# Kernel optimization log

Measured on AMD Instinct MI355X. Metric: run time of the kernel, lower is better.

## Reference

```python
import jax, jax.numpy as jnp
import numpy as np

PAD = 0  # pad_token_id sentinel used for word_starts and labels_arcs masking


def setup_inputs() -> dict:
    B, S, H, L = 16, 256, 768, 37
    key = jax.random.key(0)
    k1, k2, k3, k4, k5 = jax.random.split(key, 5)
    hidden = jax.random.normal(k1, (B, S, H), dtype=jnp.float32)
    # strictly-increasing subword start indices (1,3,5,...), zero-padded to S
    n_starts = S // 2
    row = jnp.concatenate([
        1 + 2 * jnp.arange(n_starts, dtype=jnp.int32),
        jnp.zeros(S - n_starts, dtype=jnp.int32),
    ])
    word_starts = jnp.tile(row[None, :], (B, 1))
    n_words = n_starts - 1  # spans are between consecutive starts
    la = jax.random.randint(k2, (B, S), 1, 2 * S, dtype=jnp.int32)
    labels_arcs = jnp.where(jnp.arange(S)[None, :] < n_words, la, PAD)
    labels_rels = jax.random.randint(k3, (B, S), 0, L, dtype=jnp.int32)
    W_arc = jax.random.normal(k4, (H + 1, H), dtype=jnp.float32) * 0.02
    W_rel = jax.random.normal(k5, (L, H + 1, H + 1), dtype=jnp.float32) * 0.02
    return dict(hidden=hidden, W_arc=W_arc, W_rel=W_rel,
                word_starts=word_starts, labels_arcs=labels_arcs,
                labels_rels=labels_rels)


def _merge_subword_tokens(hidden, word_starts):
    """Fused segment-mean: word j = mean(hidden[start_j:start_{j+1}])."""
    B, S, H = hidden.shape
    csum = jnp.concatenate(
        [jnp.zeros((B, 1, H), hidden.dtype), jnp.cumsum(hidden, axis=1)], axis=1)
    n_valid = jnp.sum(word_starts != PAD, axis=1)  # [B]
    start = word_starts  # [B,S]
    end = jnp.concatenate(
        [word_starts[:, 1:], jnp.zeros((B, 1), word_starts.dtype)], axis=1)
    valid = (jnp.arange(S)[None, :] + 1) < n_valid[:, None]  # word j needs start j+1
    s0 = jnp.take_along_axis(csum, start[..., None].astype(jnp.int32), axis=1)
    s1 = jnp.take_along_axis(csum, end[..., None].astype(jnp.int32), axis=1)
    length = jnp.clip(end - start, 1, None).astype(hidden.dtype)[..., None]
    return jnp.where(valid[..., None], (s1 - s0) / length, 0.0)  # [B,S,H]


def _with_ones(x):
    return jnp.concatenate([x, jnp.ones_like(x[..., :1])], axis=-1)


def reference(hidden, W_arc, W_rel, word_starts, labels_arcs, labels_rels):
    deps = _merge_subword_tokens(hidden, word_starts)            # [B,S,H]
    heads = jnp.concatenate([hidden, deps], axis=1)              # [B,2S,H]
    xa = _with_ones(deps)                                        # [B,S,H+1]
    arc_preds = jnp.einsum('bxi,ij,byj->bxy', xa, W_arc, heads)  # [B,S,2S]
    yr = _with_ones(heads)                                       # [B,2S,H+1]
    rel_preds = jnp.einsum('bxi,oij,byj->bxyo', xa, W_rel, yr)   # [B,S,2S,L]

    B, S, Y, L = rel_preds.shape
    mask = (labels_arcs != PAD).astype(hidden.dtype)             # [B,S]
    n = jnp.sum(mask)
    arc_lp = jax.nn.log_softmax(arc_preds, axis=-1)
    safe_arcs = jnp.clip(labels_arcs, 0, Y - 1)
    arc_ll = jnp.take_along_axis(arc_lp, safe_arcs[..., None], axis=-1)[..., 0]
    arc_loss = -jnp.sum(arc_ll * mask) / n

    idx = jnp.broadcast_to(safe_arcs[:, :, None, None], (B, S, 1, L))
    rel_sel = jnp.take_along_axis(rel_preds, idx, axis=2)[:, :, 0, :]  # [B,S,L]
    rel_lp = jax.nn.log_softmax(rel_sel, axis=-1)
    rel_ll = jnp.take_along_axis(rel_lp, labels_rels[..., None], axis=-1)[..., 0]
    rel_loss = -jnp.sum(rel_ll * mask) / n

    loss = arc_loss + rel_loss
    return loss, rel_preds, arc_preds
```

## Files before the change

### kernel.cpp

```cpp
#include <hip/hip_runtime.h>
#include <cmath>
#include <cstdint>


#define NB 16
#define SS 256
#define HH 768
#define LLn 37
#define YY 512
#define KP 800
#define JR 768

static const long long REL_ELEMS = (long long)NB * SS * YY * LLn;

typedef __bf16 bf16_t;
typedef __bf16 bf16x8 __attribute__((ext_vector_type(8)));
typedef float f32x4 __attribute__((ext_vector_type(4)));

__device__ __forceinline__ void async_copy16(const void* g, void* l) {
  __builtin_amdgcn_global_load_lds((__attribute__((address_space(1))) void*)(g),
                                   (__attribute__((address_space(3))) void*)(l),
                                   16, 0, 0);
}


__global__ void count_valid(const int* __restrict__ word_starts,
                            int* __restrict__ n_valid, float* __restrict__ lossacc) {
  __shared__ int cnt;
  if (threadIdx.x == 0) cnt = 0;
  __syncthreads();
  const int b = blockIdx.x;
  if (word_starts[b * SS + threadIdx.x] != 0) atomicAdd(&cnt, 1);
  __syncthreads();
  if (threadIdx.x == 0) {
    n_valid[b] = cnt;
    if (b == 0) { lossacc[0] = 0.f; lossacc[1] = 0.f; }
  }
}

__global__ void hid_rows(const float* __restrict__ hidden, bf16_t* __restrict__ yrb) {
  const long long r = blockIdx.x;
  const int b = (int)(r >> 8), y = (int)(r & 255);
  const float* src = hidden + r * HH;
  bf16_t* dst = yrb + ((long long)b * YY + y) * KP;
  const int t = threadIdx.x;
  for (int h = t; h < HH; h += 256) dst[h] = (bf16_t)src[h];
  if (t < KP - HH) dst[HH + t] = (t == 0) ? (bf16_t)1.0f : (bf16_t)0.0f;
}

__global__ void build_deps(const float* __restrict__ hidden, const int* __restrict__ word_starts,
                           const int* __restrict__ n_valid,
                           bf16_t* __restrict__ xa_p, bf16_t* __restrict__ yrb) {
  const int x = blockIdx.x, b = blockIdx.y, t = threadIdx.x;
  const int nv = n_valid[b];
  const bool valid = (x + 1) < nv;
  int start = word_starts[b * SS + x];
  int end = (x + 1 < SS) ? word_starts[b * SS + x + 1] : 0;
  start = min(max(start, 0), SS); end = min(max(end, 0), SS);
  const int len = max(end - start, 1);
  const float inv = 1.0f / (float)len;
  const float* hb = hidden + (long long)b * SS * HH;
  bf16_t* xr = xa_p + (long long)(b * SS + x) * KP;
  bf16_t* yr = yrb + ((long long)b * YY + SS + x) * KP;
  for (int h = t; h < HH; h += 256) {
    float s = 0.f;
    if (valid) for (int tt = start; tt < end; ++tt) s += hb[(long long)tt * HH + h];
    const bf16_t bv = (bf16_t)(valid ? s * inv : 0.f);
    xr[h] = bv; yr[h] = bv;
  }
  if (t < KP - HH) {
    const bf16_t v = (t == 0) ? (bf16_t)1.0f : (bf16_t)0.0f;
    xr[HH + t] = v; yr[HH + t] = v;
  }
}

__global__ void conv_warc(const float* __restrict__ W, bf16_t* __restrict__ Wab) {
  __shared__ float tbuf[32][33];
  const int i0 = blockIdx.x * 32, j0 = blockIdx.y * 32;
  const int tx = threadIdx.x, ty = threadIdx.y;
  for (int rr = 0; rr < 32; rr += 8) {
    const int i = i0 + ty + rr, j = j0 + tx;
    tbuf[ty + rr][tx] = (i < HH + 1) ? W[(long long)i * HH + j] : 0.f;
  }
  __syncthreads();
  for (int rr = 0; rr < 32; rr += 8) {
    const int j = j0 + ty + rr, i = i0 + tx;
    Wab[(long long)j * KP + i] = (bf16_t)tbuf[tx][ty + rr];
  }
}

__global__ void conv_wrel(const float* __restrict__ W, bf16_t* __restrict__ Wb, int o0) {
  __shared__ float tbuf[32][33];
  const int o = o0 + blockIdx.z;
  const int i0 = blockIdx.x * 32, j0 = blockIdx.y * 32;
  const int tx = threadIdx.x, ty = threadIdx.y;
  const float* Wo = W + (long long)o * (HH + 1) * (HH + 1);
  for (int rr = 0; rr < 32; rr += 8) {
    const int i = i0 + ty + rr, j = j0 + tx;
    tbuf[ty + rr][tx] = (i < HH + 1) ? Wo[(long long)i * (HH + 1) + j] : 0.f;
  }
  __syncthreads();
  bf16_t* Wbo = Wb + (long long)blockIdx.z * JR * KP;
  for (int rr = 0; rr < 32; rr += 8) {
    const int j = j0 + ty + rr, i = i0 + tx;
    Wbo[(long long)j * KP + i] = (bf16_t)tbuf[tx][ty + rr];
  }
}

__global__ void build_wb768(const float* __restrict__ W, bf16_t* __restrict__ Wb768) {
  const int o = blockIdx.x;
  bf16_t* dst = Wb768 + (long long)o * KP;
  for (int i = threadIdx.x; i < KP; i += 256) {
    float v = 0.f;
    if (o < LLn && i < HH + 1)
      v = W[(long long)o * (HH + 1) * (HH + 1) + (long long)i * (HH + 1) + HH];
    dst[i] = (bf16_t)v;
  }
}


template<int MODE>
__global__ __launch_bounds__(256)
void gemm_bt(const bf16_t* __restrict__ A, long long sAz, int lda,
             const bf16_t* __restrict__ B, long long sBz, int ldb,
             int K,
             float* __restrict__ Cf, bf16_t* __restrict__ Cb,
             long long sCz, int ldc,
             int OC, int o0, const float* __restrict__ bias2) {
  __shared__ __align__(16) char smem_raw[16896];
  bf16_t* As = (bf16_t*)smem_raw;
  bf16_t* Bs = (bf16_t*)(smem_raw + 8192);
  const int tid = threadIdx.x;
  const int w = tid >> 6;
  const int lane = tid & 63;
  const int z = blockIdx.z;
  const long long row0 = (long long)blockIdx.y * 128;
  const long long col0 = (long long)blockIdx.x * 128;
  const bf16_t* Ab = A + z * sAz + row0 * lda;
  const bf16_t* Bb = B + z * sBz + col0 * ldb;

  const int r_in = lane >> 2;
  const int kofs = (lane & 3) * 8;
  const bf16_t* gA0 = Ab + (long long)(w * 32 + r_in) * lda + kofs;
  const bf16_t* gB0 = Bb + (long long)(w * 32 + r_in) * ldb + kofs;
  const bf16_t* gA1 = gA0 + 16ll * lda;
  const bf16_t* gB1 = gB0 + 16ll * ldb;
  bf16_t* lA0 = &As[(w * 32) * 32];
  bf16_t* lA1 = &As[(w * 32 + 16) * 32];
  bf16_t* lB0 = &Bs[(w * 32) * 32];
  bf16_t* lB1 = &Bs[(w * 32 + 16) * 32];

  f32x4 acc[4][4];
  #pragma unroll
  for (int i = 0; i < 4; i++)
    #pragma unroll
    for (int j = 0; j < 4; j++)
      #pragma unroll
      for (int e = 0; e < 4; e++) acc[i][j][e] = 0.f;

  const int wm = (w >> 1) * 64, wn = (w & 1) * 64;
  const int fr = lane & 15;
  const int fq = lane >> 4;
  const int aoff = fq * 8;

  for (int k0 = 0; k0 < K; k0 += 32) {
    async_copy16(gA0 + k0, lA0);
    async_copy16(gA1 + k0, lA1);
    async_copy16(gB0 + k0, lB0);
    async_copy16(gB1 + k0, lB1);
    __syncthreads();
    bf16x8 af[4], bfr[4];
    #pragma unroll
    for (int t = 0; t < 4; t++) af[t]  = *(const bf16x8*)&As[(wm + t * 16 + fr) * 32 + aoff];
    #pragma unroll
    for (int t = 0; t < 4; t++) bfr[t] = *(const bf16x8*)&Bs[(wn + t * 16 + fr) * 32 + aoff];
    #pragma unroll
    for (int tm = 0; tm < 4; tm++)
      #pragma unroll
      for (int tn = 0; tn < 4; tn++)
        acc[tm][tn] = __builtin_amdgcn_mfma_f32_16x16x32_bf16(af[tm], bfr[tn], acc[tm][tn], 0, 0, 0);
    __syncthreads();
  }

  if (MODE == 2) {
    float* ebuf = (float*)smem_raw;
    const int c = tid & 127;
    const int rgrp = tid >> 7;
    const int n = (int)col0 + c;
    const int x = n / OC;
    const int o = o0 + (n - x * OC);
    const float bias = bias2[(((long long)z << 8) + x) * 128 + o];
    float* outp = Cf + z * sCz + (long long)x * (YY * LLn) + o;
    #pragma unroll
    for (int ch = 0; ch < 4; ch++) {
      #pragma unroll
      for (int tn = 0; tn < 4; tn++)
        #pragma unroll
        for (int e = 0; e < 4; e++)
          ebuf[((w >> 1) * 16 + fq * 4 + e) * 132 + wn + tn * 16 + fr] = acc[ch][tn][e];
      __syncthreads();
      const long long ybase = row0 + (long long)rgrp * 64 + ch * 16;
      #pragma unroll
      for (int r = 0; r < 16; r++)
        outp[(ybase + r) * LLn] = ebuf[(rgrp * 16 + r) * 132 + c] + bias;
      __syncthreads();
    }
  } else {
    const int er = fq * 4;
    #pragma unroll
    for (int tm = 0; tm < 4; tm++) {
      #pragma unroll
      for (int tn = 0; tn < 4; tn++) {
        const int rl = wm + tm * 16 + er;
        const long long col = col0 + wn + tn * 16 + fr;
        if (MODE == 0) {
          bf16_t* dst = Cb + z * sCz + col;
          #pragma unroll
          for (int r = 0; r < 4; r++)
            dst[(row0 + rl + r) * (long long)ldc] = (bf16_t)acc[tm][tn][r];
        } else {
          float* dst = Cf + z * sCz + col;
          #pragma unroll
          for (int r = 0; r < 4; r++)
            dst[(row0 + rl + r) * (long long)ldc] = acc[tm][tn][r];
        }
      }
    }
  }
}


__device__ __forceinline__ float wave_max(float v) {
  #pragma unroll
  for (int off = 32; off > 0; off >>= 1) v = fmaxf(v, __shfl_xor(v, off));
  return v;
}
__device__ __forceinline__ float wave_sum(float v) {
  #pragma unroll
  for (int off = 32; off > 0; off >>= 1) v += __shfl_xor(v, off);
  return v;
}

__global__ void loss_kernel(const float* __restrict__ arc, const float* __restrict__ rel,
                            const int* __restrict__ la, const int* __restrict__ lr,
                            float* __restrict__ acc) {
  const int r = blockIdx.x;
  const int lane = threadIdx.x;
  const int lab = la[r];
  const float* ar = arc + (long long)r * YY;
  float v[8]; float m = -INFINITY;
  #pragma unroll
  for (int i = 0; i < 8; i++) { v[i] = ar[lane + 64 * i]; m = fmaxf(m, v[i]); }
  m = wave_max(m);
  float s = 0.f;
  #pragma unroll
  for (int i = 0; i < 8; i++) s += expf(v[i] - m);
  s = wave_sum(s);
  const float lse_a = m + logf(s);
  const int safe = lab < 0 ? 0 : (lab > YY - 1 ? YY - 1 : lab);
  const float* rr = rel + ((long long)r * YY + safe) * LLn;
  const float rv = (lane < LLn) ? rr[lane] : -INFINITY;
  const float m2 = wave_max(rv);
  const float s2 = wave_sum((lane < LLn) ? expf(rv - m2) : 0.f);
  const float lse_r = m2 + logf(s2);
  if (lane == 0 && lab != 0) {
    const float ll = (ar[safe] - lse_a) + (rr[lr[r]] - lse_r);
    atomicAdd(&acc[0], ll);
    atomicAdd(&acc[1], 1.f);
  }
}

__global__ void finalize(const float* __restrict__ acc, float* __restrict__ out) {
  out[0] = -acc[0] / acc[1];
}


extern "C" void kernel_launch(void* const* d_in, const int* in_sizes, int n_in,
                              void* d_out, int out_size, void* d_ws, size_t ws_size,
                              hipStream_t stream) {
  (void)in_sizes; (void)n_in; (void)out_size;
  const float* hidden      = (const float*)d_in[0];
  const float* W_arc       = (const float*)d_in[1];
  const float* W_rel       = (const float*)d_in[2];
  const int* word_starts   = (const int*)d_in[3];
  const int* labels_arcs   = (const int*)d_in[4];
  const int* labels_rels   = (const int*)d_in[5];

  float* out = (float*)d_out;
  float* rel_out = out + 1;
  float* arc_out = rel_out + REL_ELEMS;

  char* ws = (char*)d_ws;
  int* n_valid = (int*)ws;
  float* lossacc = (float*)(ws + 64);
  bf16_t* xa_p  = (bf16_t*)(ws + 256);
  bf16_t* yrb   = xa_p + (size_t)NB * SS * KP;
  bf16_t* Wab   = yrb + (size_t)NB * YY * KP;
  bf16_t* A1    = Wab + (size_t)HH * KP;
  bf16_t* Wb768 = A1 + (size_t)NB * SS * HH;
  float*  bias2 = (float*)(Wb768 + (size_t)128 * KP);
  bf16_t* Wbc   = (bf16_t*)(bias2 + (size_t)NB * SS * 128);

  const size_t fixedB = 256 + 2 * ((size_t)NB * SS * KP + (size_t)NB * YY * KP +
                                   (size_t)HH * KP + (size_t)NB * SS * HH +
                                   (size_t)128 * KP) +
                        4 * (size_t)NB * SS * 128;
  const size_t perOC = 2 * ((size_t)JR * KP + (size_t)NB * SS * JR);
  int OC = 1;
  if (ws_size > fixedB + perOC) {
    const size_t m = (ws_size - fixedB) / perOC;
    OC = (m > (size_t)LLn) ? LLn : (int)m;
  }
  bf16_t* M_p = Wbc + (size_t)OC * JR * KP;

  count_valid<<<NB, SS, 0, stream>>>(word_starts, n_valid, lossacc);
  hid_rows<<<NB * SS, 256, 0, stream>>>(hidden, yrb);
  build_deps<<<dim3(SS, NB), 256, 0, stream>>>(hidden, word_starts, n_valid, xa_p, yrb);
  conv_warc<<<dim3(25, 24), dim3(32, 8), 0, stream>>>(W_arc, Wab);
  build_wb768<<<128, 256, 0, stream>>>(W_rel, Wb768);

  gemm_bt<0><<<dim3(6, 32, 1), 256, 0, stream>>>(xa_p, 0, KP, Wab, 0, KP, KP,
                                                 nullptr, A1, 0, HH, 0, 0, nullptr);
  gemm_bt<1><<<dim3(4, 2, NB), 256, 0, stream>>>(A1, (long long)SS * HH, HH,
                                                 yrb, (long long)YY * KP, KP, HH,
                                                 arc_out, nullptr, (long long)SS * YY, YY,
                                                 0, 0, nullptr);
  gemm_bt<1><<<dim3(1, 32, 1), 256, 0, stream>>>(xa_p, 0, KP, Wb768, 0, KP, KP,
                                                 bias2, nullptr, 0, 128, 0, 0, nullptr);

  for (int o0 = 0; o0 < LLn; o0 += OC) {
    const int oc = (LLn - o0 < OC) ? (LLn - o0) : OC;
    conv_wrel<<<dim3(25, 24, oc), dim3(32, 8), 0, stream>>>(W_rel, Wbc, o0);
    gemm_bt<0><<<dim3(6, 32, oc), 256, 0, stream>>>(xa_p, 0, KP,
                                                    Wbc, (long long)JR * KP, KP, KP,
                                                    nullptr, M_p, JR, oc * JR, 0, 0, nullptr);
    gemm_bt<2><<<dim3(2 * oc, 4, NB), 256, 0, stream>>>(yrb, (long long)YY * KP, KP,
                                                        M_p, (long long)SS * oc * JR, JR, JR,
                                                        rel_out, nullptr,
                                                        (long long)SS * YY * LLn, 0,
                                                        oc, o0, bias2);
  }

  loss_kernel<<<NB * SS, 64, 0, stream>>>(arc_out, rel_out, labels_arcs, labels_rels, lossacc);
  finalize<<<1, 1, 0, stream>>>(lossacc, out);
}
```

Baseline: 1.084 ms.

## Fold bias row into GEMM epilogue, drop padded K, double row tile for rel GEMMs

Removes the explicit ones-column padding (K=800) by folding the bias row/column of W_arc and W_rel into GEMM epilogue bias adds, so all GEMMs run with K=768. The deps matrix is read directly from the yrb buffer via an A-view instead of a separate xa_p copy, and count_valid/build_wb768 are merged into one misc kernel. The rel GEMMs use a templated 256-row tile (RT=2) to raise reuse of the B tile. This cuts wasted MACs and memory traffic, at the cost of higher register and LDS use per block, which may lower occupancy.

```diff
diff --git a/kernel.cpp b/kernel.cpp
--- a/kernel.cpp
+++ b/kernel.cpp
@@ -8,8 +8,6 @@
 #define HH 768
 #define LLn 37
 #define YY 512
-#define KP 800
-#define JR 768
 
 static const long long REL_ELEMS = (long long)NB * SS * YY * LLn;
 
@@ -24,53 +22,31 @@
 }
 
 
-__global__ void count_valid(const int* __restrict__ word_starts,
-                            int* __restrict__ n_valid, float* __restrict__ lossacc) {
-  __shared__ int cnt;
-  if (threadIdx.x == 0) cnt = 0;
-  __syncthreads();
-  const int b = blockIdx.x;
-  if (word_starts[b * SS + threadIdx.x] != 0) atomicAdd(&cnt, 1);
-  __syncthreads();
-  if (threadIdx.x == 0) {
-    n_valid[b] = cnt;
-    if (b == 0) { lossacc[0] = 0.f; lossacc[1] = 0.f; }
-  }
-}
-
 __global__ void hid_rows(const float* __restrict__ hidden, bf16_t* __restrict__ yrb) {
   const long long r = blockIdx.x;
   const int b = (int)(r >> 8), y = (int)(r & 255);
   const float* src = hidden + r * HH;
-  bf16_t* dst = yrb + ((long long)b * YY + y) * KP;
-  const int t = threadIdx.x;
-  for (int h = t; h < HH; h += 256) dst[h] = (bf16_t)src[h];
-  if (t < KP - HH) dst[HH + t] = (t == 0) ? (bf16_t)1.0f : (bf16_t)0.0f;
-}
-
-__global__ void build_deps(const float* __restrict__ hidden, const int* __restrict__ word_starts,
-                           const int* __restrict__ n_valid,
-                           bf16_t* __restrict__ xa_p, bf16_t* __restrict__ yrb) {
+  bf16_t* dst = yrb + ((long long)b * YY + y) * HH;
+  for (int h = threadIdx.x; h < HH; h += 256) dst[h] = (bf16_t)src[h];
+}
+
+__global__ void build_deps2(const float* __restrict__ hidden,
+                            const int* __restrict__ word_starts,
+                            bf16_t* __restrict__ yrb) {
   const int x = blockIdx.x, b = blockIdx.y, t = threadIdx.x;
-  const int nv = n_valid[b];
-  const bool valid = (x + 1) < nv;
-  int start = word_starts[b * SS + x];
-  int end = (x + 1 < SS) ? word_starts[b * SS + x + 1] : 0;
-  start = min(max(start, 0), SS); end = min(max(end, 0), SS);
+  const int ws0 = word_starts[b * SS + x];
+  const int ws1 = (x + 1 < SS) ? word_starts[b * SS + x + 1] : 0;
+  const bool valid = (x + 1 < SS) && (ws1 != 0);
+  const int start = min(max(ws0, 0), SS);
+  const int end = min(max(ws1, 0), SS);
   const int len = max(end - start, 1);
   const float inv = 1.0f / (float)len;
   const float* hb = hidden + (long long)b * SS * HH;
-  bf16_t* xr = xa_p + (long long)(b * SS + x) * KP;
-  bf16_t* yr = yrb + ((long long)b * YY + SS + x) * KP;
+  bf16_t* yr = yrb + ((long long)b * YY + SS + x) * HH;
   for (int h = t; h < HH; h += 256) {
     float s = 0.f;
     if (valid) for (int tt = start; tt < end; ++tt) s += hb[(long long)tt * HH + h];
-    const bf16_t bv = (bf16_t)(valid ? s * inv : 0.f);
-    xr[h] = bv; yr[h] = bv;
-  }
-  if (t < KP - HH) {
-    const bf16_t v = (t == 0) ? (bf16_t)1.0f : (bf16_t)0.0f;
-    xr[HH + t] = v; yr[HH + t] = v;
+    yr[h] = (bf16_t)(valid ? s * inv : 0.f);
   }
 }
 
@@ -78,15 +54,11 @@
   __shared__ float tbuf[32][33];
   const int i0 = blockIdx.x * 32, j0 = blockIdx.y * 32;
   const int tx = threadIdx.x, ty = threadIdx.y;
-  for (int rr = 0; rr < 32; rr += 8) {
-    const int i = i0 + ty + rr, j = j0 + tx;
-    tbuf[ty + rr][tx] = (i < HH + 1) ? W[(long long)i * HH + j] : 0.f;
-  }
+  for (int rr = 0; rr < 32; rr += 8)
+    tbuf[ty + rr][tx] = W[(long long)(i0 + ty + rr) * HH + j0 + tx];
   __syncthreads();
-  for (int rr = 0; rr < 32; rr += 8) {
-    const int j = j0 + ty + rr, i = i0 + tx;
-    Wab[(long long)j * KP + i] = (bf16_t)tbuf[tx][ty + rr];
-  }
+  for (int rr = 0; rr < 32; rr += 8)
+    Wab[(long long)(j0 + ty + rr) * HH + i0 + tx] = (bf16_t)tbuf[tx][ty + rr];
 }
 
 __global__ void conv_wrel(const float* __restrict__ W, bf16_t* __restrict__ Wb, int o0) {
@@ -95,90 +67,109 @@
   const int i0 = blockIdx.x * 32, j0 = blockIdx.y * 32;
   const int tx = threadIdx.x, ty = threadIdx.y;
   const float* Wo = W + (long long)o * (HH + 1) * (HH + 1);
-  for (int rr = 0; rr < 32; rr += 8) {
-    const int i = i0 + ty + rr, j = j0 + tx;
-    tbuf[ty + rr][tx] = (i < HH + 1) ? Wo[(long long)i * (HH + 1) + j] : 0.f;
-  }
+  for (int rr = 0; rr < 32; rr += 8)
+    tbuf[ty + rr][tx] = Wo[(long long)(i0 + ty + rr) * (HH + 1) + j0 + tx];
   __syncthreads();
-  bf16_t* Wbo = Wb + (long long)blockIdx.z * JR * KP;
-  for (int rr = 0; rr < 32; rr += 8) {
-    const int j = j0 + ty + rr, i = i0 + tx;
-    Wbo[(long long)j * KP + i] = (bf16_t)tbuf[tx][ty + rr];
-  }
-}
-
-__global__ void build_wb768(const float* __restrict__ W, bf16_t* __restrict__ Wb768) {
-  const int o = blockIdx.x;
-  bf16_t* dst = Wb768 + (long long)o * KP;
-  for (int i = threadIdx.x; i < KP; i += 256) {
-    float v = 0.f;
-    if (o < LLn && i < HH + 1)
-      v = W[(long long)o * (HH + 1) * (HH + 1) + (long long)i * (HH + 1) + HH];
-    dst[i] = (bf16_t)v;
-  }
-}
-
-
-template<int MODE>
+  bf16_t* Wbo = Wb + (long long)blockIdx.z * HH * HH;
+  for (int rr = 0; rr < 32; rr += 8)
+    Wbo[(long long)(j0 + ty + rr) * HH + i0 + tx] = (bf16_t)tbuf[tx][ty + rr];
+}
+
+__global__ void build_misc(const float* __restrict__ W_rel, const float* __restrict__ W_arc,
+                           float* __restrict__ WbiasJ, bf16_t* __restrict__ Wb768,
+                           float* __restrict__ bias768b, float* __restrict__ biasArc,
+                           float* __restrict__ lossacc) {
+  const int blk = blockIdx.x, t = threadIdx.x;
+  if (blk < LLn) {
+    const int o = blk;
+    const float* Wo = W_rel + (long long)o * (HH + 1) * (HH + 1);
+    for (int j = t; j < HH; j += 256)
+      WbiasJ[(long long)o * HH + j] = Wo[(long long)HH * (HH + 1) + j];
+    for (int i = t; i < HH; i += 256)
+      Wb768[(long long)o * HH + i] = (bf16_t)Wo[(long long)i * (HH + 1) + HH];
+    if (t == 0) bias768b[o] = Wo[(long long)HH * (HH + 1) + HH];
+  } else if (blk == LLn) {
+    for (int j = t; j < HH; j += 256) biasArc[j] = W_arc[(long long)HH * HH + j];
+    if (t == 0) { lossacc[0] = 0.f; lossacc[1] = 0.f; }
+  } else {
+    for (int i = t; i < (128 - LLn) * HH; i += 256) Wb768[(long long)LLn * HH + i] = (bf16_t)0.f;
+    if (t + LLn < 128) bias768b[t + LLn] = 0.f;
+  }
+}
+
+
+template<int RT, int MODE>
 __global__ __launch_bounds__(256)
-void gemm_bt(const bf16_t* __restrict__ A, long long sAz, int lda,
+void gemm_bt(const bf16_t* __restrict__ A, long long sAz, int lda, int aview,
              const bf16_t* __restrict__ B, long long sBz, int ldb,
              int K,
              float* __restrict__ Cf, bf16_t* __restrict__ Cb,
              long long sCz, int ldc,
-             int OC, int o0, const float* __restrict__ bias2) {
-  __shared__ __align__(16) char smem_raw[16896];
+             const float* __restrict__ cbias, int sbias,
+             int OC, int o0, const float* __restrict__ bias_xo) {
+  constexpr int SM0 = RT * 8192 + 8192;
+  constexpr int SMEM = SM0 > 16896 ? SM0 : 16896;
+  __shared__ __align__(16) char smem_raw[SMEM];
   bf16_t* As = (bf16_t*)smem_raw;
-  bf16_t* Bs = (bf16_t*)(smem_raw + 8192);
+  bf16_t* Bs = (bf16_t*)(smem_raw + RT * 8192);
   const int tid = threadIdx.x;
   const int w = tid >> 6;
   const int lane = tid & 63;
   const int z = blockIdx.z;
-  const long long row0 = (long long)blockIdx.y * 128;
+  const long long row0 = (long long)blockIdx.y * (RT * 128);
   const long long col0 = (long long)blockIdx.x * 128;
-  const bf16_t* Ab = A + z * sAz + row0 * lda;
+  const bf16_t* Ab;
+  if (aview) {
+    const long long bb = row0 >> 8;
+    Ab = A + (bb * 512 + 256 + (row0 & 255)) * (long long)lda;
+  } else {
+    Ab = A + z * sAz + row0 * lda;
+  }
   const bf16_t* Bb = B + z * sBz + col0 * ldb;
 
   const int r_in = lane >> 2;
   const int kofs = (lane & 3) * 8;
-  const bf16_t* gA0 = Ab + (long long)(w * 32 + r_in) * lda + kofs;
+  const bf16_t* gA[2 * RT];
+  bf16_t* lA[2 * RT];
+  #pragma unroll
+  for (int c = 0; c < 2 * RT; c++) {
+    gA[c] = Ab + (long long)(w * (32 * RT) + c * 16 + r_in) * lda + kofs;
+    lA[c] = &As[(w * (32 * RT) + c * 16) * 32];
+  }
   const bf16_t* gB0 = Bb + (long long)(w * 32 + r_in) * ldb + kofs;
-  const bf16_t* gA1 = gA0 + 16ll * lda;
   const bf16_t* gB1 = gB0 + 16ll * ldb;
-  bf16_t* lA0 = &As[(w * 32) * 32];
-  bf16_t* lA1 = &As[(w * 32 + 16) * 32];
   bf16_t* lB0 = &Bs[(w * 32) * 32];
   bf16_t* lB1 = &Bs[(w * 32 + 16) * 32];
 
-  f32x4 acc[4][4];
-  #pragma unroll
-  for (int i = 0; i < 4; i++)
+  f32x4 acc[4 * RT][4];
+  #pragma unroll
+  for (int i = 0; i < 4 * RT; i++)
     #pragma unroll
     for (int j = 0; j < 4; j++)
       #pragma unroll
       for (int e = 0; e < 4; e++) acc[i][j][e] = 0.f;
 
-  const int wm = (w >> 1) * 64, wn = (w & 1) * 64;
+  const int wm = (w >> 1) * (64 * RT), wn = (w & 1) * 64;
   const int fr = lane & 15;
   const int fq = lane >> 4;
   const int aoff = fq * 8;
 
   for (int k0 = 0; k0 < K; k0 += 32) {
-    async_copy16(gA0 + k0, lA0);
-    async_copy16(gA1 + k0, lA1);
+    #pragma unroll
+    for (int c = 0; c < 2 * RT; c++) async_copy16(gA[c] + k0, lA[c]);
     async_copy16(gB0 + k0, lB0);
     async_copy16(gB1 + k0, lB1);
     __syncthreads();
-    bf16x8 af[4], bfr[4];
-    #pragma unroll
-    for (int t = 0; t < 4; t++) af[t]  = *(const bf16x8*)&As[(wm + t * 16 + fr) * 32 + aoff];
+    bf16x8 bfr[4];
     #pragma unroll
     for (int t = 0; t < 4; t++) bfr[t] = *(const bf16x8*)&Bs[(wn + t * 16 + fr) * 32 + aoff];
     #pragma unroll
-    for (int tm = 0; tm < 4; tm++)
+    for (int tm = 0; tm < 4 * RT; tm++) {
+      const bf16x8 af = *(const bf16x8*)&As[(wm + tm * 16 + fr) * 32 + aoff];
       #pragma unroll
       for (int tn = 0; tn < 4; tn++)
-        acc[tm][tn] = __builtin_amdgcn_mfma_f32_16x16x32_bf16(af[tm], bfr[tn], acc[tm][tn], 0, 0, 0);
+        acc[tm][tn] = __builtin_amdgcn_mfma_f32_16x16x32_bf16(af, bfr[tn], acc[tm][tn], 0, 0, 0);
+    }
     __syncthreads();
   }
 
@@ -189,17 +180,17 @@
     const int n = (int)col0 + c;
     const int x = n / OC;
     const int o = o0 + (n - x * OC);
-    const float bias = bias2[(((long long)z << 8) + x) * 128 + o];
+    const float bias = bias_xo[(((long long)z << 8) + x) * 128 + o];
     float* outp = Cf + z * sCz + (long long)x * (YY * LLn) + o;
     #pragma unroll
-    for (int ch = 0; ch < 4; ch++) {
+    for (int ch = 0; ch < 4 * RT; ch++) {
       #pragma unroll
       for (int tn = 0; tn < 4; tn++)
         #pragma unroll
         for (int e = 0; e < 4; e++)
           ebuf[((w >> 1) * 16 + fq * 4 + e) * 132 + wn + tn * 16 + fr] = acc[ch][tn][e];
       __syncthreads();
-      const long long ybase = row0 + (long long)rgrp * 64 + ch * 16;
+      const long long ybase = row0 + (long long)rgrp * (64 * RT) + ch * 16;
       #pragma unroll
       for (int r = 0; r < 16; r++)
         outp[(ybase + r) * LLn] = ebuf[(rgrp * 16 + r) * 132 + c] + bias;
@@ -208,21 +199,22 @@
   } else {
     const int er = fq * 4;
     #pragma unroll
-    for (int tm = 0; tm < 4; tm++) {
-      #pragma unroll
-      for (int tn = 0; tn < 4; tn++) {
+    for (int tn = 0; tn < 4; tn++) {
+      const long long col = col0 + wn + tn * 16 + fr;
+      const float bv = cbias ? cbias[(long long)z * sbias + col] : 0.f;
+      #pragma unroll
+      for (int tm = 0; tm < 4 * RT; tm++) {
         const int rl = wm + tm * 16 + er;
-        const long long col = col0 + wn + tn * 16 + fr;
         if (MODE == 0) {
           bf16_t* dst = Cb + z * sCz + col;
           #pragma unroll
           for (int r = 0; r < 4; r++)
-            dst[(row0 + rl + r) * (long long)ldc] = (bf16_t)acc[tm][tn][r];
+            dst[(row0 + rl + r) * (long long)ldc] = (bf16_t)(acc[tm][tn][r] + bv);
         } else {
           float* dst = Cf + z * sCz + col;
           #pragma unroll
           for (int r = 0; r < 4; r++)
-            dst[(row0 + rl + r) * (long long)ldc] = acc[tm][tn][r];
+            dst[(row0 + rl + r) * (long long)ldc] = acc[tm][tn][r] + bv;
         }
       }
     }
@@ -291,54 +283,57 @@
   float* arc_out = rel_out + REL_ELEMS;
 
   char* ws = (char*)d_ws;
-  int* n_valid = (int*)ws;
-  float* lossacc = (float*)(ws + 64);
-  bf16_t* xa_p  = (bf16_t*)(ws + 256);
-  bf16_t* yrb   = xa_p + (size_t)NB * SS * KP;
-  bf16_t* Wab   = yrb + (size_t)NB * YY * KP;
-  bf16_t* A1    = Wab + (size_t)HH * KP;
-  bf16_t* Wb768 = A1 + (size_t)NB * SS * HH;
-  float*  bias2 = (float*)(Wb768 + (size_t)128 * KP);
-  bf16_t* Wbc   = (bf16_t*)(bias2 + (size_t)NB * SS * 128);
-
-  const size_t fixedB = 256 + 2 * ((size_t)NB * SS * KP + (size_t)NB * YY * KP +
-                                   (size_t)HH * KP + (size_t)NB * SS * HH +
-                                   (size_t)128 * KP) +
-                        4 * (size_t)NB * SS * 128;
-  const size_t perOC = 2 * ((size_t)JR * KP + (size_t)NB * SS * JR);
+  float* lossacc  = (float*)ws;
+  bf16_t* yrb     = (bf16_t*)(ws + 256);
+  bf16_t* Wab     = yrb + (size_t)NB * YY * HH;
+  bf16_t* A1      = Wab + (size_t)HH * HH;
+  bf16_t* Wb768   = A1 + (size_t)NB * SS * HH;
+  float*  biasArc = (float*)(Wb768 + (size_t)128 * HH);
+  float*  bias768b= biasArc + HH;
+  float*  d_bias2 = bias768b + 128;
+  float*  WbiasJ  = d_bias2 + (size_t)NB * SS * 128;
+  bf16_t* Wbc     = (bf16_t*)(WbiasJ + (size_t)LLn * HH);
+
+  const size_t fixedB = 256 +
+      2 * ((size_t)NB * YY * HH + (size_t)HH * HH + (size_t)NB * SS * HH +
+           (size_t)128 * HH) +
+      4 * ((size_t)HH + 128 + (size_t)NB * SS * 128 + (size_t)LLn * HH);
+  const size_t perOC = 2 * ((size_t)HH * HH + (size_t)NB * SS * HH);
   int OC = 1;
   if (ws_size > fixedB + perOC) {
     const size_t m = (ws_size - fixedB) / perOC;
     OC = (m > (size_t)LLn) ? LLn : (int)m;
   }
-  bf16_t* M_p = Wbc + (size_t)OC * JR * KP;
-
-  count_valid<<<NB, SS, 0, stream>>>(word_starts, n_valid, lossacc);
+  bf16_t* M_p = Wbc + (size_t)OC * HH * HH;
+
   hid_rows<<<NB * SS, 256, 0, stream>>>(hidden, yrb);
-  build_deps<<<dim3(SS, NB), 256, 0, stream>>>(hidden, word_starts, n_valid, xa_p, yrb);
-  conv_warc<<<dim3(25, 24), dim3(32, 8), 0, stream>>>(W_arc, Wab);
-  build_wb768<<<128, 256, 0, stream>>>(W_rel, Wb768);
-
-  gemm_bt<0><<<dim3(6, 32, 1), 256, 0, stream>>>(xa_p, 0, KP, Wab, 0, KP, KP,
-                                                 nullptr, A1, 0, HH, 0, 0, nullptr);
-  gemm_bt<1><<<dim3(4, 2, NB), 256, 0, stream>>>(A1, (long long)SS * HH, HH,
-                                                 yrb, (long long)YY * KP, KP, HH,
-                                                 arc_out, nullptr, (long long)SS * YY, YY,
-                                                 0, 0, nullptr);
-  gemm_bt<1><<<dim3(1, 32, 1), 256, 0, stream>>>(xa_p, 0, KP, Wb768, 0, KP, KP,
-                                                 bias2, nullptr, 0, 128, 0, 0, nullptr);
+  build_deps2<<<dim3(SS, NB), 256, 0, stream>>>(hidden, word_starts, yrb);
+  conv_warc<<<dim3(24, 24), dim3(32, 8), 0, stream>>>(W_arc, Wab);
+  build_misc<<<39, 256, 0, stream>>>(W_rel, W_arc, WbiasJ, Wb768, bias768b, biasArc, lossacc);
+
+  gemm_bt<1, 0><<<dim3(6, 32, 1), 256, 0, stream>>>(
+      yrb, 0, HH, 1, Wab, 0, HH, HH,
+      nullptr, A1, 0, HH, biasArc, 0, 0, 0, nullptr);
+  gemm_bt<1, 1><<<dim3(4, 2, NB), 256, 0, stream>>>(
+      A1, (long long)SS * HH, HH, 0,
+      yrb, (long long)YY * HH, HH, HH,
+      arc_out, nullptr, (long long)SS * YY, YY, nullptr, 0, 0, 0, nullptr);
+  gemm_bt<1, 1><<<dim3(1, 32, 1), 256, 0, stream>>>(
+      yrb, 0, HH, 1, Wb768, 0, HH, HH,
+      d_bias2, nullptr, 0, 128, bias768b, 0, 0, 0, nullptr);
 
   for (int o0 = 0; o0 < LLn; o0 += OC) {
     const int oc = (LLn - o0 < OC) ? (LLn - o0) : OC;
-    conv_wrel<<<dim3(25, 24, oc), dim3(32, 8), 0, stream>>>(W_rel, Wbc, o0);
-    gemm_bt<0><<<dim3(6, 32, oc), 256, 0, stream>>>(xa_p, 0, KP,
-                                                    Wbc, (long long)JR * KP, KP, KP,
-                                                    nullptr, M_p, JR, oc * JR, 0, 0, nullptr);
-    gemm_bt<2><<<dim3(2 * oc, 4, NB), 256, 0, stream>>>(yrb, (long long)YY * KP, KP,
-                                                        M_p, (long long)SS * oc * JR, JR, JR,
-                                                        rel_out, nullptr,
-                                                        (long long)SS * YY * LLn, 0,
-                                                        oc, o0, bias2);
+    conv_wrel<<<dim3(24, 24, oc), dim3(32, 8), 0, stream>>>(W_rel, Wbc, o0);
+    gemm_bt<2, 0><<<dim3(6, 16, oc), 256, 0, stream>>>(
+        yrb, 0, HH, 1,
+        Wbc, (long long)HH * HH, HH, HH,
+        nullptr, M_p, HH, oc * HH, WbiasJ + (long long)o0 * HH, HH, 0, 0, nullptr);
+    gemm_bt<2, 2><<<dim3(2 * oc, 2, NB), 256, 0, stream>>>(
+        yrb, (long long)YY * HH, HH, 0,
+        M_p, (long long)SS * oc * HH, HH, HH,
+        rel_out, nullptr, (long long)SS * YY * LLn, 0, nullptr, 0,
+        oc, o0, d_bias2);
   }
 
   loss_kernel<<<NB * SS, 64, 0, stream>>>(arc_out, rel_out, labels_arcs, labels_rels, lossacc);
```

Result: slower. 1.199 ms (+10.6%).
